# Optimization experiments

Hardware: AMD Instinct MI355X
Metric: run time of the kernel (lower is better)

Reference implementation:

```python
import jax, jax.numpy as jnp
import numpy as np

NUM_EXPERTS = 64
NOISE_STD = 1.0
CAPACITY = 32  # top-C items per expert (experts-choice routing)
D_MODEL = 512
NUM_GROUPS = 8
GROUP_SIZE = 2048


def _top_items_per_expert_dispatcher(gates):
    """Experts-choice dispatcher for one group.

    gates: (S, E) softmax gate values.
    Returns:
      dispatch: (E, C, S) one-hot selection of the top-C items per expert.
      combine:  (S, E, C) gate value if item s is expert e's c-th pick, else 0.
    """
    s = gates.shape[0]
    # Each expert picks its top-C items by gate value.
    _, top_idx = jax.lax.top_k(gates.T, CAPACITY)          # (E, C)
    dispatch = jax.nn.one_hot(top_idx, s, dtype=gates.dtype)  # (E, C, S)
    combine = jnp.einsum('se,ecs->sec', gates, dispatch)      # (S, E, C)
    return dispatch, combine


def setup_inputs() -> dict:
    key = jax.random.key(0)
    k1, k2 = jax.random.split(key)
    inputs = jax.random.normal(k1, (NUM_GROUPS, GROUP_SIZE, D_MODEL), dtype=jnp.float32)
    # Dense(num_experts, use_bias=False) kernel, lecun-normal-ish scale.
    W = jax.random.normal(k2, (D_MODEL, NUM_EXPERTS), dtype=jnp.float32) * (D_MODEL ** -0.5)
    return {"inputs": inputs, "W": W}


def reference(inputs, W):
    # Gating projection: (G, S, D) x (D, E) -> (G, S, E)
    logits = jnp.einsum('gsd,de->gse', inputs, W)
    # Noisy gating: noise_std scaled by 1/num_experts (as in the module).
    noise_scale = NOISE_STD / NUM_EXPERTS
    noise = noise_scale * jax.random.normal(jax.random.key(42), logits.shape, dtype=logits.dtype)
    gates = jax.nn.softmax(logits + noise, axis=-1)  # (G, S, E)
    # vmap the per-group top-items-per-expert dispatcher over groups.
    dispatch, combine = jax.vmap(_top_items_per_expert_dispatcher)(gates)
    return combine, dispatch
```

## Files before the change

kernel.cpp:

```cpp
#include <hip/hip_runtime.h>
#include <math.h>
#include <stdint.h>

#define NG 8
#define GS 2048
#define DM 512
#define NE 64
#define CAP 32
#define NROWS (NG * GS)
#define COMBINE_ELEMS (33554432ull)

#define GATE_BLOCKS 512
#define XSTc 68
#define CHW (32 * XSTc)
#define TBS 21

typedef float f32x4 __attribute__((ext_vector_type(4)));
typedef double f64x2 __attribute__((ext_vector_type(2)));
typedef double f64x4 __attribute__((ext_vector_type(4)));
typedef unsigned long long u64;

__device__ __forceinline__ void threefry2x32(uint32_t k0, uint32_t k1,
                                             uint32_t x0, uint32_t x1,
                                             uint32_t& o0, uint32_t& o1) {
  uint32_t ks[3] = {k0, k1, k0 ^ k1 ^ 0x1BD11BDAu};
  x0 += ks[0];
  x1 += ks[1];
  const uint32_t rot[2][4] = {{13u, 15u, 26u, 6u}, {17u, 29u, 16u, 24u}};
#pragma unroll
  for (int i = 0; i < 5; ++i) {
#pragma unroll
    for (int j = 0; j < 4; ++j) {
      uint32_t r = rot[i & 1][j];
      x0 += x1;
      x1 = (x1 << r) | (x1 >> (32u - r));
      x1 ^= x0;
    }
    x0 += ks[(i + 1) % 3];
    x1 += ks[(i + 2) % 3] + (uint32_t)(i + 1);
  }
  o0 = x0;
  o1 = x1;
}

__device__ __forceinline__ float erfinv_xla(float x) {
  float w = -log1pf(-x * x);
  float p;
  if (w < 5.0f) {
    w = w - 2.5f;
    p = 2.81022636e-08f;
    p = __fmaf_rn(p, w, 3.43273939e-07f);
    p = __fmaf_rn(p, w, -3.5233877e-06f);
    p = __fmaf_rn(p, w, -4.39150654e-06f);
    p = __fmaf_rn(p, w, 0.00021858087f);
    p = __fmaf_rn(p, w, -0.00125372503f);
    p = __fmaf_rn(p, w, -0.00417768164f);
    p = __fmaf_rn(p, w, 0.246640727f);
    p = __fmaf_rn(p, w, 1.50140941f);
  } else {
    w = sqrtf(w) - 3.0f;
    p = -0.000200214257f;
    p = __fmaf_rn(p, w, 0.000100950558f);
    p = __fmaf_rn(p, w, 0.00134934322f);
    p = __fmaf_rn(p, w, -0.00367342844f);
    p = __fmaf_rn(p, w, 0.00573950773f);
    p = __fmaf_rn(p, w, -0.0076224613f);
    p = __fmaf_rn(p, w, 0.00943887047f);
    p = __fmaf_rn(p, w, 1.00167406f);
    p = __fmaf_rn(p, w, 2.83297682f);
  }
  return p * x;
}

__device__ __forceinline__ float jax_normal(uint32_t idx) {
  uint32_t o0, o1;
  threefry2x32(0u, 42u, 0u, idx, o0, o1);
  uint32_t bits = o0 ^ o1;
  float f = __uint_as_float((bits >> 9) | 0x3f800000u) - 1.0f;
  const float lo = __uint_as_float(0xBF7FFFFFu);
  float v = fmaxf(lo, f * 2.0f + lo);
  return __uint_as_float(0x3FB504F3u) * erfinv_xla(v);
}

__global__ __launch_bounds__(256) void wprep_kernel(
    const float* __restrict__ Wt, double* __restrict__ Wd) {
  const int i = blockIdx.x * 256 + threadIdx.x;
  const int t = i & 3, i15 = (i >> 2) & 15, row = i >> 6;
  Wd[i] = (double)Wt[row * NE + t * 16 + i15];
}

__global__ __launch_bounds__(256) void gate_kernel(
    const float* __restrict__ x,
    const double* __restrict__ Wd,
    float* __restrict__ gatesT) {
  __shared__ float xs[2 * CHW];
  __shared__ double pd[128 * 16];
  const int gid = blockIdx.x;
  const int tid = threadIdx.x;
  const int l = tid & 63;
  const int w4 = tid >> 6;
  const int wr = w4 & 1;
  const int kh = w4 >> 1;
  const int row0b = gid * 32;
  const int row0 = row0b + wr * 16;

  const int i15 = l & 15;
  const int k4 = l >> 4;

  f64x4 dr = {0., 0., 0., 0.};
  dr = __builtin_amdgcn_mfma_f64_16x16x4f64((double)i15, 0.25, dr, 0, 0, 0);
  int perm[4];
#pragma unroll
  for (int r = 0; r < 4; ++r) perm[r] = ((int)(dr[r] + 0.5)) & 15;

  const int sr0 = tid >> 4, sc0 = (tid & 15) << 2;
  const int sr1 = (tid + 256) >> 4, sc1 = ((tid + 256) & 15) << 2;
  const float* xg0 = x + (size_t)(row0b + sr0) * DM + sc0;
  const float* xg1 = x + (size_t)(row0b + sr1) * DM + sc1;
  float* xl0 = xs + sr0 * XSTc + sc0;
  float* xl1 = xs + sr1 * XSTc + sc1;

  {
    const f32x4 a0 = *(const f32x4*)xg0;
    const f32x4 a1 = *(const f32x4*)xg1;
    *(f32x4*)xl0 = a0;
    *(f32x4*)xl1 = a1;
  }
  __syncthreads();

  f64x4 acc[4] = {{0., 0., 0., 0.}, {0., 0., 0., 0.},
                  {0., 0., 0., 0.}, {0., 0., 0., 0.}};
  const int abase = (wr * 16 + i15) * XSTc + k4;
  const int kl0 = kh * 8;
  for (int ck = 0; ck < 8; ++ck) {
    const int cur = ck & 1;
    f32x4 a0, a1;
    const bool more = (ck < 7);
    if (more) {
      a0 = *(const f32x4*)(xg0 + (ck + 1) * 64);
      a1 = *(const f32x4*)(xg1 + (ck + 1) * 64);
    }
    const float* ar = xs + cur * CHW + abase;
#pragma unroll
    for (int kkl = 0; kkl < 8; ++kkl) {
      const int kloc = kl0 + kkl;
      const double a = (double)ar[kloc * 4];
      const int kk = ck * 16 + kloc;
      const double* wrow = Wd + ((size_t)((kk << 2) + k4)) * 64 + i15 * 4;
      const f64x2 b01 = *(const f64x2*)(wrow + 0);
      const f64x2 b23 = *(const f64x2*)(wrow + 2);
      acc[0] = __builtin_amdgcn_mfma_f64_16x16x4f64(a, b01[0], acc[0], 0, 0, 0);
      acc[1] = __builtin_amdgcn_mfma_f64_16x16x4f64(a, b01[1], acc[1], 0, 0, 0);
      acc[2] = __builtin_amdgcn_mfma_f64_16x16x4f64(a, b23[0], acc[2], 0, 0, 0);
      acc[3] = __builtin_amdgcn_mfma_f64_16x16x4f64(a, b23[1], acc[3], 0, 0, 0);
    }
    if (more) {
      float* d0 = xs + (cur ^ 1) * CHW + sr0 * XSTc + sc0;
      float* d1 = xs + (cur ^ 1) * CHW + sr1 * XSTc + sc1;
      *(f32x4*)d0 = a0;
      *(f32x4*)d1 = a1;
    }
    __syncthreads();
  }

  if (kh == 1) {
    double* dst = pd + ((size_t)(wr * 64 + l)) * 16;
#pragma unroll
    for (int t = 0; t < 4; ++t)
#pragma unroll
      for (int r = 0; r < 4; ++r) dst[t * 4 + r] = acc[t][r];
  }
  __syncthreads();
  if (kh == 1) return;

  {
    const double* src = pd + ((size_t)(wr * 64 + l)) * 16;
#pragma unroll
    for (int t = 0; t < 4; ++t)
#pragma unroll
      for (int r = 0; r < 4; ++r) acc[t][r] += src[t * 4 + r];
  }

  float gatef[4][4];
#pragma unroll
  for (int r = 0; r < 4; ++r) {
    const int row = row0 + perm[r];
    double v[4];
    double m = -1.0e300;
#pragma unroll
    for (int t = 0; t < 4; ++t) {
      const float logit = (float)acc[t][r];
      const float noised =
          logit + 0.015625f * jax_normal((uint32_t)(row * NE + 16 * t + i15));
      v[t] = (double)noised;
      m = fmax(m, v[t]);
    }
#pragma unroll
    for (int off = 1; off < 16; off <<= 1) m = fmax(m, __shfl_xor(m, off, 64));
    double s = 0.0;
#pragma unroll
    for (int t = 0; t < 4; ++t) {
      v[t] = exp(v[t] - m);
      s += v[t];
    }
#pragma unroll
    for (int off = 1; off < 16; off <<= 1) s += __shfl_xor(s, off, 64);
#pragma unroll
    for (int t = 0; t < 4; ++t) gatef[t][r] = (float)(v[t] / s);
  }

  float* tb = xs + wr * (NE * TBS);
#pragma unroll
  for (int t = 0; t < 4; ++t)
#pragma unroll
    for (int r = 0; r < 4; ++r)
      tb[(16 * t + i15) * TBS + perm[r]] = gatef[t][r];

  const int g = row0 >> 11;
  const int s0 = row0 & (GS - 1);
  float* drow = gatesT + ((size_t)(g * NE + l)) * GS + s0;
#pragma unroll
  for (int c = 0; c < 4; ++c) {
    f32x4 o;
#pragma unroll
    for (int i = 0; i < 4; ++i) o[i] = tb[l * TBS + 4 * c + i];
    *(f32x4*)&drow[4 * c] = o;
  }
}

__global__ __launch_bounds__(256) void topwrite_kernel(
    const float* __restrict__ gatesT,
    float* __restrict__ out) {
  __shared__ u64 keys[CAP];
  __shared__ int sel_s[CAP];
  __shared__ float sel_v[CAP];
  __shared__ unsigned char c_of_s[GS];
  const int ge = blockIdx.x;
  const int g = ge >> 6, e = ge & 63;
  const int tid = threadIdx.x;
  const int lane = tid & 63, w = tid >> 6;

  ((u64*)c_of_s)[tid] = ~0ull;

  if (w == 0) {
    const float* base = gatesT + (size_t)ge * GS;
    u64 K[32];
#pragma unroll
    for (int k = 0; k < 8; ++k) {
      const f32x4 t = *(const f32x4*)(base + k * 256 + lane * 4);
#pragma unroll
      for (int i = 0; i < 4; ++i) {
        const int s = k * 256 + lane * 4 + i;
        K[k * 4 + i] = ((u64)__float_as_uint(t[i]) << 32) | (u64)(2047 - s);
      }
    }
#pragma unroll
    for (int k = 2; k <= 32; k <<= 1) {
#pragma unroll
      for (int d = k >> 1; d > 0; d >>= 1) {
#pragma unroll
        for (int j = 0; j < 32; ++j) {
          const int ixj = j ^ d;
          if (ixj > j) {
            const bool asc = ((j & k) == 0);
            const u64 a = K[j], b = K[ixj];
            const bool sw = asc ? (a > b) : (a < b);
            K[j] = sw ? b : a;
            K[ixj] = sw ? a : b;
          }
        }
      }
    }
#pragma unroll
    for (int m = 1; m < 64; m <<= 1) {
      u64 tmp[32];
#pragma unroll
      for (int j = 0; j < 32; ++j) tmp[j] = __shfl_xor(K[31 - j], m, 64);
#pragma unroll
      for (int j = 0; j < 32; ++j) K[j] = (K[j] > tmp[j]) ? K[j] : tmp[j];
#pragma unroll
      for (int d = 16; d > 0; d >>= 1) {
#pragma unroll
        for (int j = 0; j < 32; ++j) {
          if ((j & d) == 0) {
            const u64 a = K[j], b = K[j | d];
            const bool sw = (a > b);
            K[j] = sw ? b : a;
            K[j | d] = sw ? a : b;
          }
        }
      }
    }
#pragma unroll
    for (int c = 0; c < CAP; ++c) {
      if (lane == c) keys[c] = K[31 - c];
    }
  }
  __syncthreads();

  if (tid < CAP) {
    const u64 key = keys[tid];
    sel_s[tid] = 2047 - (int)(key & 0x7FFull);
    sel_v[tid] = __uint_as_float((uint32_t)(key >> 32));
  }
  __syncthreads();
  if (tid < CAP) c_of_s[sel_s[tid]] = (unsigned char)tid;
  __syncthreads();

  float* drow_base = out + COMBINE_ELEMS + (size_t)ge * CAP * GS;
#pragma unroll
  for (int rr = 0; rr < 8; ++rr) {
    const int c = 8 * w + rr;
    const int sc = sel_s[c];
    float* rowp = drow_base + (size_t)c * GS;
#pragma unroll
    for (int j = 0; j < 8; ++j) {
      const int pos = j * 256 + lane * 4;
      f32x4 v;
      v[0] = (sc == pos + 0) ? 1.0f : 0.0f;
      v[1] = (sc == pos + 1) ? 1.0f : 0.0f;
      v[2] = (sc == pos + 2) ? 1.0f : 0.0f;
      v[3] = (sc == pos + 3) ? 1.0f : 0.0f;
      *(f32x4*)&rowp[pos] = v;
    }
  }

  const int pos = (lane & 7) * 4;
  for (int it = 0; it < 64; ++it) {
    const int s = 512 * w + 8 * it + (lane >> 3);
    const int c = c_of_s[s];
    const float val = (c != 255) ? sel_v[c & 31] : 0.0f;
    const int d = c - pos;
    f32x4 v;
    v[0] = (d == 0) ? val : 0.0f;
    v[1] = (d == 1) ? val : 0.0f;
    v[2] = (d == 2) ? val : 0.0f;
    v[3] = (d == 3) ? val : 0.0f;
    *(f32x4*)&out[(((size_t)(g * GS + s)) * NE + e) * CAP + pos] = v;
  }
}

extern "C" void kernel_launch(void* const* d_in, const int* in_sizes, int n_in,
                              void* d_out, int out_size, void* d_ws,
                              size_t ws_size, hipStream_t stream) {
  (void)in_sizes; (void)n_in; (void)ws_size; (void)out_size;
  const float* x = (const float*)d_in[0];
  const float* Wt = (const float*)d_in[1];
  float* out = (float*)d_out;
  float* gatesT = (float*)d_ws;
  double* Wd = (double*)((char*)d_ws + ((size_t)NROWS * NE * 4));

  wprep_kernel<<<128, 256, 0, stream>>>(Wt, Wd);
  gate_kernel<<<GATE_BLOCKS, 256, 0, stream>>>(x, Wd, gatesT);
  topwrite_kernel<<<NG * NE, 256, 0, stream>>>(gatesT, out);
}
```

Before: 105.1 us.

## Split top-k selection from output writes to make combine stores contiguous

```diff
diff --git a/kernel.cpp b/kernel.cpp
--- a/kernel.cpp
+++ b/kernel.cpp
@@ -228,115 +228,123 @@
   }
 }
 
-__global__ __launch_bounds__(256) void topwrite_kernel(
+__global__ __launch_bounds__(64) void topsel_kernel(
     const float* __restrict__ gatesT,
-    float* __restrict__ out) {
-  __shared__ u64 keys[CAP];
-  __shared__ int sel_s[CAP];
-  __shared__ float sel_v[CAP];
-  __shared__ unsigned char c_of_s[GS];
+    u64* __restrict__ topsel) {
   const int ge = blockIdx.x;
-  const int g = ge >> 6, e = ge & 63;
-  const int tid = threadIdx.x;
-  const int lane = tid & 63, w = tid >> 6;
-
-  ((u64*)c_of_s)[tid] = ~0ull;
-
-  if (w == 0) {
-    const float* base = gatesT + (size_t)ge * GS;
-    u64 K[32];
-#pragma unroll
-    for (int k = 0; k < 8; ++k) {
-      const f32x4 t = *(const f32x4*)(base + k * 256 + lane * 4);
-#pragma unroll
-      for (int i = 0; i < 4; ++i) {
-        const int s = k * 256 + lane * 4 + i;
-        K[k * 4 + i] = ((u64)__float_as_uint(t[i]) << 32) | (u64)(2047 - s);
-      }
-    }
-#pragma unroll
-    for (int k = 2; k <= 32; k <<= 1) {
-#pragma unroll
-      for (int d = k >> 1; d > 0; d >>= 1) {
-#pragma unroll
-        for (int j = 0; j < 32; ++j) {
-          const int ixj = j ^ d;
-          if (ixj > j) {
-            const bool asc = ((j & k) == 0);
-            const u64 a = K[j], b = K[ixj];
-            const bool sw = asc ? (a > b) : (a < b);
-            K[j] = sw ? b : a;
-            K[ixj] = sw ? a : b;
-          }
+  const int lane = threadIdx.x;
+
+  const float* base = gatesT + (size_t)ge * GS;
+  u64 K[32];
+#pragma unroll
+  for (int k = 0; k < 8; ++k) {
+    const f32x4 t = *(const f32x4*)(base + k * 256 + lane * 4);
+#pragma unroll
+    for (int i = 0; i < 4; ++i) {
+      const int s = k * 256 + lane * 4 + i;
+      K[k * 4 + i] = ((u64)__float_as_uint(t[i]) << 32) | (u64)(2047 - s);
+    }
+  }
+
+#pragma unroll
+  for (int k = 2; k <= 32; k <<= 1) {
+#pragma unroll
+    for (int d = k >> 1; d > 0; d >>= 1) {
+#pragma unroll
+      for (int j = 0; j < 32; ++j) {
+        const int ixj = j ^ d;
+        if (ixj > j) {
+          const bool asc = ((j & k) == 0);
+          const u64 a = K[j], b = K[ixj];
+          const bool sw = asc ? (a > b) : (a < b);
+          K[j] = sw ? b : a;
+          K[ixj] = sw ? a : b;
         }
       }
     }
-#pragma unroll
-    for (int m = 1; m < 64; m <<= 1) {
-      u64 tmp[32];
-#pragma unroll
-      for (int j = 0; j < 32; ++j) tmp[j] = __shfl_xor(K[31 - j], m, 64);
-#pragma unroll
-      for (int j = 0; j < 32; ++j) K[j] = (K[j] > tmp[j]) ? K[j] : tmp[j];
-#pragma unroll
-      for (int d = 16; d > 0; d >>= 1) {
-#pragma unroll
-        for (int j = 0; j < 32; ++j) {
-          if ((j & d) == 0) {
-            const u64 a = K[j], b = K[j | d];
-            const bool sw = (a > b);
-            K[j] = sw ? b : a;
-            K[j | d] = sw ? a : b;
-          }
+  }
+
+#pragma unroll
+  for (int m = 1; m < 64; m <<= 1) {
+    u64 tmp[32];
+#pragma unroll
+    for (int j = 0; j < 32; ++j) tmp[j] = __shfl_xor(K[31 - j], m, 64);
+#pragma unroll
+    for (int j = 0; j < 32; ++j) K[j] = (K[j] > tmp[j]) ? K[j] : tmp[j];
+#pragma unroll
+    for (int d = 16; d > 0; d >>= 1) {
+#pragma unroll
+      for (int j = 0; j < 32; ++j) {
+        if ((j & d) == 0) {
+          const u64 a = K[j], b = K[j | d];
+          const bool sw = (a > b);
+          K[j] = sw ? b : a;
+          K[j | d] = sw ? a : b;
         }
       }
     }
-#pragma unroll
-    for (int c = 0; c < CAP; ++c) {
-      if (lane == c) keys[c] = K[31 - c];
-    }
-  }
-  __syncthreads();
-
-  if (tid < CAP) {
-    const u64 key = keys[tid];
-    sel_s[tid] = 2047 - (int)(key & 0x7FFull);
-    sel_v[tid] = __uint_as_float((uint32_t)(key >> 32));
-  }
-  __syncthreads();
-  if (tid < CAP) c_of_s[sel_s[tid]] = (unsigned char)tid;
-  __syncthreads();
-
-  float* drow_base = out + COMBINE_ELEMS + (size_t)ge * CAP * GS;
-#pragma unroll
-  for (int rr = 0; rr < 8; ++rr) {
-    const int c = 8 * w + rr;
-    const int sc = sel_s[c];
-    float* rowp = drow_base + (size_t)c * GS;
-#pragma unroll
-    for (int j = 0; j < 8; ++j) {
-      const int pos = j * 256 + lane * 4;
-      f32x4 v;
-      v[0] = (sc == pos + 0) ? 1.0f : 0.0f;
-      v[1] = (sc == pos + 1) ? 1.0f : 0.0f;
-      v[2] = (sc == pos + 2) ? 1.0f : 0.0f;
-      v[3] = (sc == pos + 3) ? 1.0f : 0.0f;
-      *(f32x4*)&rowp[pos] = v;
-    }
-  }
-
-  const int pos = (lane & 7) * 4;
-  for (int it = 0; it < 64; ++it) {
-    const int s = 512 * w + 8 * it + (lane >> 3);
-    const int c = c_of_s[s];
-    const float val = (c != 255) ? sel_v[c & 31] : 0.0f;
-    const int d = c - pos;
-    f32x4 v;
-    v[0] = (d == 0) ? val : 0.0f;
-    v[1] = (d == 1) ? val : 0.0f;
-    v[2] = (d == 2) ? val : 0.0f;
-    v[3] = (d == 3) ? val : 0.0f;
-    *(f32x4*)&out[(((size_t)(g * GS + s)) * NE + e) * CAP + pos] = v;
+  }
+
+#pragma unroll
+  for (int c = 0; c < CAP; ++c) {
+    if (lane == c) topsel[(size_t)ge * CAP + c] = K[31 - c];
+  }
+}
+
+__global__ __launch_bounds__(256) void outwrite_kernel(
+    const u64* __restrict__ topsel,
+    float* __restrict__ out) {
+  __shared__ int sel_s[CAP];
+  const int bid = blockIdx.x;
+  const int tid = threadIdx.x;
+
+  if (bid < 2048) {
+    const int g = bid >> 8;
+    const int s0 = (bid & 255) * 8;
+    f32x4* dst = (f32x4*)(out + ((size_t)(g * GS + s0)) * NE * CAP);
+    const f32x4 z = {0.f, 0.f, 0.f, 0.f};
+#pragma unroll
+    for (int j = 0; j < 16; ++j) dst[j * 256 + tid] = z;
+    __syncthreads();
+
+    const int e = tid >> 2;
+    const int c0 = (tid & 3) * 8;
+    const u64* tp = topsel + ((size_t)(g * NE + e)) * CAP + c0;
+#pragma unroll
+    for (int i = 0; i < 8; ++i) {
+      const u64 key = tp[i];
+      const int s_sel = 2047 - (int)(key & 0x7FFull);
+      if (s_sel >= s0 && s_sel < s0 + 8) {
+        const float v = __uint_as_float((uint32_t)(key >> 32));
+        out[(((size_t)(g * GS + s_sel)) * NE + e) * CAP + c0 + i] = v;
+      }
+    }
+  } else {
+    const int ge = bid - 2048;
+    const int lane = tid & 63, w = tid >> 6;
+    if (tid < CAP) {
+      const u64 key = topsel[(size_t)ge * CAP + tid];
+      sel_s[tid] = 2047 - (int)(key & 0x7FFull);
+    }
+    __syncthreads();
+
+    float* drow_base = out + COMBINE_ELEMS + (size_t)ge * CAP * GS;
+#pragma unroll
+    for (int rr = 0; rr < 8; ++rr) {
+      const int c = 8 * w + rr;
+      const int sc = sel_s[c];
+      float* rowp = drow_base + (size_t)c * GS;
+#pragma unroll
+      for (int j = 0; j < 8; ++j) {
+        const int pos = j * 256 + lane * 4;
+        f32x4 v;
+        v[0] = (sc == pos + 0) ? 1.0f : 0.0f;
+        v[1] = (sc == pos + 1) ? 1.0f : 0.0f;
+        v[2] = (sc == pos + 2) ? 1.0f : 0.0f;
+        v[3] = (sc == pos + 3) ? 1.0f : 0.0f;
+        *(f32x4*)&rowp[pos] = v;
+      }
+    }
   }
 }
 
@@ -349,8 +357,10 @@
   float* out = (float*)d_out;
   float* gatesT = (float*)d_ws;
   double* Wd = (double*)((char*)d_ws + ((size_t)NROWS * NE * 4));
+  u64* topsel = (u64*)((char*)Wd + (size_t)DM * NE * 8);
 
   wprep_kernel<<<128, 256, 0, stream>>>(Wt, Wd);
   gate_kernel<<<GATE_BLOCKS, 256, 0, stream>>>(x, Wd, gatesT);
-  topwrite_kernel<<<NG * NE, 256, 0, stream>>>(gatesT, out);
-}
+  topsel_kernel<<<NG * NE, 64, 0, stream>>>(gatesT, topsel);
+  outwrite_kernel<<<2560, 256, 0, stream>>>(topsel, out);
+}
```

Result: slower. 108.1 us (+2.8%).
